# Kernel tuning notes

Measured on AMD Instinct MI355X. Metric: run time of the kernel, lower is better.

The kernel has to match this reference:

```python
import jax, jax.numpy as jnp
import numpy as np

D_MODEL = 1024
NUM_HEADS = 16
D_K = D_MODEL // NUM_HEADS
ROPE_BASE = 10000.0


def _rotate_half(x):
    # interleaved pairs: (x0, x1) -> (-x1, x0)
    x1 = x[..., ::2]
    x2 = x[..., 1::2]
    return jnp.stack((-x2, x1), axis=-1).reshape(x.shape)


def _rope(q, k):
    seq_len = q.shape[-2]
    freqs = ROPE_BASE ** (jnp.arange(0, D_K, 2, dtype=q.dtype) / D_K)  # [D_K/2]
    angles = jnp.arange(seq_len, dtype=q.dtype)[:, None] / freqs[None, :]  # [S, D_K/2]
    sin = jnp.repeat(jnp.sin(angles), 2, axis=-1)[None, None]  # [1,1,S,D_K]
    cos = jnp.repeat(jnp.cos(angles), 2, axis=-1)[None, None]
    return q * cos + _rotate_half(q) * sin, k * cos + _rotate_half(k) * sin


def setup_inputs() -> dict:
    key = jax.random.key(0)
    ks = jax.random.split(key, 9)
    B, S, D = 2, 2048, D_MODEL
    s = 1.0 / np.sqrt(D)
    inp = {
        "x": jax.random.normal(ks[0], (B, S, D), dtype=jnp.float32),
        "wq": jax.random.uniform(ks[1], (D, D), jnp.float32, -s, s),
        "bq": jax.random.uniform(ks[2], (D,), jnp.float32, -s, s),
        "wk": jax.random.uniform(ks[3], (D, D), jnp.float32, -s, s),
        "bk": jax.random.uniform(ks[4], (D,), jnp.float32, -s, s),
        "wv": jax.random.uniform(ks[5], (D, D), jnp.float32, -s, s),
        "bv": jax.random.uniform(ks[6], (D,), jnp.float32, -s, s),
        "wo": jax.random.uniform(ks[7], (D, D), jnp.float32, -s, s),
        "bo": jax.random.uniform(ks[8], (D,), jnp.float32, -s, s),
    }
    return inp


def reference(x, wq, bq, wk, bk, wv, bv, wo, bo):
    B, S, D = x.shape
    H, dk = NUM_HEADS, D_K
    # torch Linear: y = x @ W.T + b
    Q = (x @ wq.T + bq).reshape(B, S, H, dk).transpose(0, 2, 1, 3)  # [B,H,S,dk]
    K = (x @ wk.T + bk).reshape(B, S, H, dk).transpose(0, 2, 1, 3)
    V = (x @ wv.T + bv).reshape(B, S, H, dk).transpose(0, 2, 1, 3)
    Q, K = _rope(Q, K)
    score = jnp.einsum("bhqd,bhkd->bhqk", Q, K) / jnp.sqrt(jnp.asarray(dk, x.dtype))
    attn_w = jax.nn.softmax(score, axis=-1)
    out = jnp.einsum("bhqk,bhkd->bhqd", attn_w, V)  # [B,H,S,dk]
    out = out.transpose(0, 2, 1, 3).reshape(B, S, D)
    return out @ wo.T + bo
```

## Files before the change

### kernel.cpp

```cpp
#include <hip/hip_runtime.h>
#include <hip/hip_bf16.h>
#include <math.h>

typedef __bf16 bf16_t;
typedef __bf16 bf16x4_t __attribute__((ext_vector_type(4)));
typedef __bf16 bf16x8_t __attribute__((ext_vector_type(8)));
typedef float  f32x4_t  __attribute__((ext_vector_type(4)));

#define SEQ 2048
#define DM  1024
#define NH  16
#define DK  64
#define ROPE_C 0.4152410118609203f
#define EXP_C (1.4426950408889634f / 8.0f)

#define GLD16(gp, lp) \
  __builtin_amdgcn_global_load_lds((__attribute__((address_space(1))) const void*)(gp), \
                                   (__attribute__((address_space(3))) void*)(lp), 16, 0, 0)

__global__ __launch_bounds__(256)
void prep_kernel(const float* __restrict__ x,  const float* __restrict__ wq,
                 const float* __restrict__ wk, const float* __restrict__ wv,
                 const float* __restrict__ wo, bf16_t* __restrict__ dst,
                 float2* __restrict__ lut) {
  if (blockIdx.x < 8192) {
    int i = blockIdx.x * 256 + threadIdx.x;
    const float* s;
    if (i < 1048576) {
      s = x + (size_t)i * 4;
    } else {
      int j = i - 1048576;
      int w = j >> 18;
      const float* base = (w == 0) ? wq : (w == 1) ? wk : (w == 2) ? wv : wo;
      s = base + (size_t)(j & 262143) * 4;
    }
    float4 v = *(const float4*)s;
    bf16x4_t o;
    o.x = (bf16_t)v.x; o.y = (bf16_t)v.y; o.z = (bf16_t)v.z; o.w = (bf16_t)v.w;
    ((bf16x4_t*)dst)[i] = o;
  } else {
    int i = (blockIdx.x - 8192) * 256 + threadIdx.x;
    int s = i >> 5, f = i & 31;
    float ang = (float)s * exp2f(-ROPE_C * (float)f);
    float sn, cs;
    sincosf(ang, &sn, &cs);
    lut[i] = make_float2(sn, cs);
  }
}

__global__ __launch_bounds__(256, 3)
void gemm_qkv(const bf16_t* __restrict__ A, const bf16_t* __restrict__ Wq,
              const bf16_t* __restrict__ Wk, const bf16_t* __restrict__ Wv,
              const float* __restrict__ bq, const float* __restrict__ bk,
              const float* __restrict__ bv, const float2* __restrict__ lut,
              bf16_t* __restrict__ Qb, bf16_t* __restrict__ Kb,
              bf16_t* __restrict__ Vtb) {
  const int K = 1024;
  __shared__ bf16_t As[128 * 64];
  __shared__ bf16_t Bs[128 * 64];

  const int tid  = threadIdx.x;
  const int w    = tid >> 6;
  const int lane = tid & 63;
  const int quad = lane >> 4;
  const int lrow = lane & 15;
  const int wm = (w >> 1) * 64, wn = (w & 1) * 64;

  const int srow8 = lane >> 3;
  const int scolz = (((lane & 7) ^ (lane >> 3)) * 8);

  const int id   = blockIdx.x;
  const int xcd  = id & 7;
  const int rank = id >> 3;
  const int isV  = rank >= 64;

  const bf16_t* Ablk;
  const bf16_t* Bblk;
  int bmQK = 0, bnl = 0, isK = 0, bmF = 0, bnT = 0;
  if (!isV) {
    const int q = xcd * 64 + rank;
    bmQK = q >> 4;
    const int bn = q & 15;
    isK = bn >> 3;
    bnl = bn & 7;
    Ablk = A + (size_t)(bmQK * 128) * K;
    Bblk = (isK ? Wk : Wq) + (size_t)(bnl * 128) * K;
  } else {
    const int v = xcd * 32 + (rank - 64);
    bnT = v >> 3;
    bmF = v & 7;
    Ablk = Wv + (size_t)(bmF * 128) * K;
    Bblk = A + (size_t)(bnT * 128) * K;
  }

  f32x4_t acc[4][4] = {};

  for (int k0 = 0; k0 < K; k0 += 64) {
#pragma unroll
    for (int i = 0; i < 4; i++) {
      GLD16(&Ablk[(size_t)(w * 32 + i * 8 + srow8) * K + k0 + scolz], &As[(w * 32 + i * 8) * 64]);
      GLD16(&Bblk[(size_t)(w * 32 + i * 8 + srow8) * K + k0 + scolz], &Bs[(w * 32 + i * 8) * 64]);
    }
    __syncthreads();

#pragma unroll
    for (int kk = 0; kk < 2; kk++) {
      const int gsw = (((kk << 2) | quad) ^ (lrow & 7)) * 8;
      bf16x8_t af[4], bf[4];
#pragma unroll
      for (int mi = 0; mi < 4; mi++)
        af[mi] = *(const bf16x8_t*)(&As[(wm + mi * 16 + lrow) * 64 + gsw]);
#pragma unroll
      for (int ni = 0; ni < 4; ni++)
        bf[ni] = *(const bf16x8_t*)(&Bs[(wn + ni * 16 + lrow) * 64 + gsw]);
#pragma unroll
      for (int mi = 0; mi < 4; mi++)
#pragma unroll
        for (int ni = 0; ni < 4; ni++)
          acc[mi][ni] = __builtin_amdgcn_mfma_f32_16x16x32_bf16(af[mi], bf[ni], acc[mi][ni], 0, 0, 0);
    }
    __syncthreads();
  }

  if (!isV) {
    const int brow = bmQK * 128 + wm;
    const int cbase = bnl * 128 + wn;
    const float* bias = isK ? bk : bq;
    bf16_t* D = isK ? Kb : Qb;

#pragma unroll
    for (int ni = 0; ni < 4; ni++) {
      const int col = cbase + ni * 16 + lrow;
      const float bvv = bias[col];
      const int t = col & 63;
      const int h = col >> 6;
      const int fidx = t >> 1;
#pragma unroll
      for (int mi = 0; mi < 4; mi++) {
        f32x4_t v = acc[mi][ni];
#pragma unroll
        for (int r = 0; r < 4; r++) {
          const int row = brow + mi * 16 + quad * 4 + r;
          const int s = row & (SEQ - 1);
          float val = v[r] + bvv;
          const float2 sc = lut[s * 32 + fidx];
          const float pv = __shfl_xor(val, 1);
          val = (t & 1) ? (val * sc.y + pv * sc.x) : (val * sc.y - pv * sc.x);
          const int b = row >> 11;
          const size_t o = (((size_t)(b * NH + h) * SEQ) + s) * DK + t;
          D[o] = (bf16_t)val;
        }
      }
    }
  } else {
    const int fbase = bmF * 128 + wm;
    const int tbase = bnT * 128 + wn;

#pragma unroll
    for (int ni = 0; ni < 4; ni++) {
      const int t = tbase + ni * 16 + lrow;
      const int b = t >> 11;
      const int s = t & (SEQ - 1);
#pragma unroll
      for (int mi = 0; mi < 4; mi++) {
        f32x4_t v = acc[mi][ni];
        const int f = fbase + mi * 16 + quad * 4;
        const int h = f >> 6, d = f & 63;
#pragma unroll
        for (int r = 0; r < 4; r++)
          Vtb[((size_t)((b * NH + h) * DK + d + r)) * SEQ + s] = (bf16_t)(v[r] + bv[f + r]);
      }
    }
  }
}

__global__ __launch_bounds__(256)
void gemm_out(const bf16_t* __restrict__ A, const bf16_t* __restrict__ Bw,
              const float* __restrict__ bias, float* __restrict__ D) {
  const int K = 1024;
  __shared__ bf16_t As[128 * 64];
  __shared__ bf16_t Bs[64 * 64];

  const int tid  = threadIdx.x;
  const int w    = tid >> 6;
  const int lane = tid & 63;
  const int quad = lane >> 4;
  const int lrow = lane & 15;
  const int wm = (w >> 1) * 64, wn = (w & 1) * 32;

  const int srow8 = lane >> 3;
  const int scolz = (((lane & 7) ^ (lane >> 3)) * 8);

  const int id  = blockIdx.x;
  const int swz = (id & 7) * 64 + (id >> 3);
  const int bm  = swz >> 4;
  const int bn  = swz & 15;

  const bf16_t* Ablk = A  + (size_t)(bm * 128) * K;
  const bf16_t* Bblk = Bw + (size_t)(bn * 64) * K;

  f32x4_t acc[4][2] = {};

  for (int k0 = 0; k0 < K; k0 += 64) {
#pragma unroll
    for (int i = 0; i < 4; i++)
      GLD16(&Ablk[(size_t)(w * 32 + i * 8 + srow8) * K + k0 + scolz], &As[(w * 32 + i * 8) * 64]);
#pragma unroll
    for (int i = 0; i < 2; i++)
      GLD16(&Bblk[(size_t)(w * 16 + i * 8 + srow8) * K + k0 + scolz], &Bs[(w * 16 + i * 8) * 64]);
    __syncthreads();

#pragma unroll
    for (int kk = 0; kk < 2; kk++) {
      const int gsw = (((kk << 2) | quad) ^ (lrow & 7)) * 8;
      bf16x8_t af[4], bf[2];
#pragma unroll
      for (int mi = 0; mi < 4; mi++)
        af[mi] = *(const bf16x8_t*)(&As[(wm + mi * 16 + lrow) * 64 + gsw]);
#pragma unroll
      for (int ni = 0; ni < 2; ni++)
        bf[ni] = *(const bf16x8_t*)(&Bs[(wn + ni * 16 + lrow) * 64 + gsw]);
#pragma unroll
      for (int mi = 0; mi < 4; mi++)
#pragma unroll
        for (int ni = 0; ni < 2; ni++)
          acc[mi][ni] = __builtin_amdgcn_mfma_f32_16x16x32_bf16(af[mi], bf[ni], acc[mi][ni], 0, 0, 0);
    }
    __syncthreads();
  }

#pragma unroll
  for (int ni = 0; ni < 2; ni++) {
    const int col = bn * 64 + wn + ni * 16 + lrow;
    const float bvv = bias[col];
#pragma unroll
    for (int mi = 0; mi < 4; mi++) {
      f32x4_t v = acc[mi][ni];
#pragma unroll
      for (int r = 0; r < 4; r++) {
        const int row = bm * 128 + wm + mi * 16 + quad * 4 + r;
        D[(size_t)row * DM + col] = v[r] + bvv;
      }
    }
  }
}

__global__ __launch_bounds__(256, 2)
void attn_kernel(const bf16_t* __restrict__ Q, const bf16_t* __restrict__ K,
                 const bf16_t* __restrict__ Vt, bf16_t* __restrict__ AO) {
  __shared__ bf16_t Ks[128 * 64];
  __shared__ bf16_t Vs[64 * 128];

  const int tid  = threadIdx.x;
  const int w    = tid >> 6;
  const int lane = tid & 63;
  const int quad = lane >> 4;
  const int lrow = lane & 15;

  const int id  = blockIdx.x;
  const int swz = (id & 7) * 64 + (id >> 3);
  const int bh  = swz >> 4;
  const int q0  = (swz & 15) * 128 + w * 32;

  const bf16_t* Qh  = Q  + (size_t)bh * SEQ * DK;
  const bf16_t* Kh  = K  + (size_t)bh * SEQ * DK;
  const bf16_t* Vth = Vt + (size_t)bh * DK * SEQ;

  bf16x8_t qfA[2], qfB[2];
#pragma unroll
  for (int c = 0; c < 2; c++) {
    bf16x8_t ta = *(const bf16x8_t*)(&Qh[(size_t)(q0 + lrow) * DK + c * 32 + quad * 8]);
    bf16x8_t tb = *(const bf16x8_t*)(&Qh[(size_t)(q0 + 16 + lrow) * DK + c * 32 + quad * 8]);
#pragma unroll
    for (int i = 0; i < 8; i++) {
      ta[i] = (bf16_t)((float)ta[i] * EXP_C);
      tb[i] = (bf16_t)((float)tb[i] * EXP_C);
    }
    qfA[c] = ta; qfB[c] = tb;
  }

  f32x4_t accA[4] = {}, accB[4] = {};
  float lsumA = 0.f, lsumB = 0.f;

  const int krow = tid >> 1;
  const int kcol = (tid & 1) * 32;
  const int kg0  = (tid & 1) * 4;
  const int ksw  = krow & 7;
  const int kwr  = krow * 64;
  const int kw0 = kwr + (((kg0 + 0) ^ ksw) << 3);
  const int kw1 = kwr + (((kg0 + 1) ^ ksw) << 3);
  const int kw2 = kwr + (((kg0 + 2) ^ ksw) << 3);
  const int kw3 = kwr + (((kg0 + 3) ^ ksw) << 3);

  const int vrow = tid >> 2;
  const int vcol = (tid & 3) * 32;
  const int vG   = (tid & 3) * 4;
  const int vsw  = vrow & 15;
  const int vwr  = vrow * 128;
  const int vw0 = vwr + (((vG + 0) ^ vsw) << 3);
  const int vw1 = vwr + (((vG + 1) ^ vsw) << 3);
  const int vw2 = vwr + (((vG + 2) ^ vsw) << 3);
  const int vw3 = vwr + (((vG + 3) ^ vsw) << 3);

  uint4 kr0 = *(const uint4*)(&Kh[(size_t)krow * DK + kcol]);
  uint4 kr1 = *(const uint4*)(&Kh[(size_t)krow * DK + kcol + 8]);
  uint4 kr2 = *(const uint4*)(&Kh[(size_t)krow * DK + kcol + 16]);
  uint4 kr3 = *(const uint4*)(&Kh[(size_t)krow * DK + kcol + 24]);
  uint4 vr0 = *(const uint4*)(&Vth[(size_t)vrow * SEQ + vcol]);
  uint4 vr1 = *(const uint4*)(&Vth[(size_t)vrow * SEQ + vcol + 8]);
  uint4 vr2 = *(const uint4*)(&Vth[(size_t)vrow * SEQ + vcol + 16]);
  uint4 vr3 = *(const uint4*)(&Vth[(size_t)vrow * SEQ + vcol + 24]);

  for (int kt = 0; kt < SEQ / 128; ++kt) {
    *(uint4*)(&Ks[kw0]) = kr0;
    *(uint4*)(&Ks[kw1]) = kr1;
    *(uint4*)(&Ks[kw2]) = kr2;
    *(uint4*)(&Ks[kw3]) = kr3;
    *(uint2*)(&Vs[vw0])     = make_uint2(vr0.x, vr0.y);
    *(uint2*)(&Vs[vw1])     = make_uint2(vr0.z, vr0.w);
    *(uint2*)(&Vs[vw2])     = make_uint2(vr1.x, vr1.y);
    *(uint2*)(&Vs[vw3])     = make_uint2(vr1.z, vr1.w);
    *(uint2*)(&Vs[vw0 + 4]) = make_uint2(vr2.x, vr2.y);
    *(uint2*)(&Vs[vw1 + 4]) = make_uint2(vr2.z, vr2.w);
    *(uint2*)(&Vs[vw2 + 4]) = make_uint2(vr3.x, vr3.y);
    *(uint2*)(&Vs[vw3 + 4]) = make_uint2(vr3.z, vr3.w);
    __syncthreads();

    if (kt + 1 < SEQ / 128) {
      const int kb = (kt + 1) * 128;
      kr0 = *(const uint4*)(&Kh[(size_t)(kb + krow) * DK + kcol]);
      kr1 = *(const uint4*)(&Kh[(size_t)(kb + krow) * DK + kcol + 8]);
      kr2 = *(const uint4*)(&Kh[(size_t)(kb + krow) * DK + kcol + 16]);
      kr3 = *(const uint4*)(&Kh[(size_t)(kb + krow) * DK + kcol + 24]);
      vr0 = *(const uint4*)(&Vth[(size_t)vrow * SEQ + kb + vcol]);
      vr1 = *(const uint4*)(&Vth[(size_t)vrow * SEQ + kb + vcol + 8]);
      vr2 = *(const uint4*)(&Vth[(size_t)vrow * SEQ + kb + vcol + 16]);
      vr3 = *(const uint4*)(&Vth[(size_t)vrow * SEQ + kb + vcol + 24]);
    }

    __builtin_amdgcn_s_setprio(1);
#pragma unroll
    for (int c2 = 0; c2 < 4; ++c2) {
      uint2 pkA[2], pkB[2];
#pragma unroll
      for (int kk2 = 0; kk2 < 2; ++kk2) {
        const int kk = c2 * 2 + kk2;
        const int krd = (kk * 16 + lrow) * 64;
        bf16x8_t kf0 = *(const bf16x8_t*)(&Ks[krd + ((quad       ^ (lrow & 7)) << 3)]);
        bf16x8_t kf1 = *(const bf16x8_t*)(&Ks[krd + (((quad + 4) ^ (lrow & 7)) << 3)]);
        f32x4_t zA = {}, zB = {};
        zA = __builtin_amdgcn_mfma_f32_16x16x32_bf16(kf0, qfA[0], zA, 0, 0, 0);
        zA = __builtin_amdgcn_mfma_f32_16x16x32_bf16(kf1, qfA[1], zA, 0, 0, 0);
        zB = __builtin_amdgcn_mfma_f32_16x16x32_bf16(kf0, qfB[0], zB, 0, 0, 0);
        zB = __builtin_amdgcn_mfma_f32_16x16x32_bf16(kf1, qfB[1], zB, 0, 0, 0);
        const float a0 = __builtin_amdgcn_exp2f(zA[0]), a1 = __builtin_amdgcn_exp2f(zA[1]);
        const float a2 = __builtin_amdgcn_exp2f(zA[2]), a3 = __builtin_amdgcn_exp2f(zA[3]);
        const float b0 = __builtin_amdgcn_exp2f(zB[0]), b1 = __builtin_amdgcn_exp2f(zB[1]);
        const float b2 = __builtin_amdgcn_exp2f(zB[2]), b3 = __builtin_amdgcn_exp2f(zB[3]);
        lsumA += (a0 + a1) + (a2 + a3);
        lsumB += (b0 + b1) + (b2 + b3);
        pkA[kk2].x = __builtin_amdgcn_perm(__builtin_bit_cast(unsigned, a1),
                                           __builtin_bit_cast(unsigned, a0), 0x07060302u);
        pkA[kk2].y = __builtin_amdgcn_perm(__builtin_bit_cast(unsigned, a3),
                                           __builtin_bit_cast(unsigned, a2), 0x07060302u);
        pkB[kk2].x = __builtin_amdgcn_perm(__builtin_bit_cast(unsigned, b1),
                                           __builtin_bit_cast(unsigned, b0), 0x07060302u);
        pkB[kk2].y = __builtin_amdgcn_perm(__builtin_bit_cast(unsigned, b3),
                                           __builtin_bit_cast(unsigned, b2), 0x07060302u);
      }
      uint4 pfuA, pfuB;
      pfuA.x = pkA[0].x; pfuA.y = pkA[0].y; pfuA.z = pkA[1].x; pfuA.w = pkA[1].y;
      pfuB.x = pkB[0].x; pfuB.y = pkB[0].y; pfuB.z = pkB[1].x; pfuB.w = pkB[1].y;
      bf16x8_t pfA = __builtin_bit_cast(bf16x8_t, pfuA);
      bf16x8_t pfB = __builtin_bit_cast(bf16x8_t, pfuB);
#pragma unroll
      for (int nt = 0; nt < 4; ++nt) {
        bf16x8_t vf = *(const bf16x8_t*)(
            &Vs[(nt * 16 + lrow) * 128 + ((((c2 << 2) | quad) ^ lrow) << 3)]);
        accA[nt] = __builtin_amdgcn_mfma_f32_16x16x32_bf16(pfA, vf, accA[nt], 0, 0, 0);
        accB[nt] = __builtin_amdgcn_mfma_f32_16x16x32_bf16(pfB, vf, accB[nt], 0, 0, 0);
      }
    }
    __builtin_amdgcn_s_setprio(0);
    __syncthreads();
  }

  lsumA += __shfl_xor(lsumA, 16);
  lsumA += __shfl_xor(lsumA, 32);
  lsumB += __shfl_xor(lsumB, 16);
  lsumB += __shfl_xor(lsumB, 32);
  float linvA[4], linvB[4];
#pragma unroll
  for (int r = 0; r < 4; r++) {
    linvA[r] = 1.0f / __shfl(lsumA, quad * 4 + r);
    linvB[r] = 1.0f / __shfl(lsumB, quad * 4 + r);
  }

  const int b = bh >> 4, h = bh & 15;
#pragma unroll
  for (int nt = 0; nt < 4; nt++)
#pragma unroll
    for (int r = 0; r < 4; r++) {
      const int rowA = q0 + quad * 4 + r;
      const int rowB = q0 + 16 + quad * 4 + r;
      const float va = accA[nt][r] * linvA[r];
      const float vb = accB[nt][r] * linvB[r];
      AO[((size_t)(b * SEQ + rowA)) * DM + h * DK + nt * 16 + lrow] = (bf16_t)va;
      AO[((size_t)(b * SEQ + rowB)) * DM + h * DK + nt * 16 + lrow] = (bf16_t)vb;
    }
}

extern "C" void kernel_launch(void* const* d_in, const int* in_sizes, int n_in,
                              void* d_out, int out_size, void* d_ws, size_t ws_size,
                              hipStream_t stream) {
  const float* x  = (const float*)d_in[0];
  const float* wq = (const float*)d_in[1];
  const float* bq = (const float*)d_in[2];
  const float* wk = (const float*)d_in[3];
  const float* bk = (const float*)d_in[4];
  const float* wv = (const float*)d_in[5];
  const float* bv = (const float*)d_in[6];
  const float* wo = (const float*)d_in[7];
  const float* bo = (const float*)d_in[8];
  float* out = (float*)d_out;

  char* ws = (char*)d_ws;
  bf16_t* xb   = (bf16_t*)(ws);
  bf16_t* wqb  = (bf16_t*)(ws + 8388608);
  bf16_t* wkb  = (bf16_t*)(ws + 10485760);
  bf16_t* wvb  = (bf16_t*)(ws + 12582912);
  bf16_t* wob  = (bf16_t*)(ws + 14680064);
  bf16_t* Qb   = (bf16_t*)(ws + 16777216);
  bf16_t* Kb   = (bf16_t*)(ws + 25165824);
  bf16_t* Vtb  = (bf16_t*)(ws + 33554432);
  bf16_t* AOb  = (bf16_t*)(ws + 41943040);
  float2* lut  = (float2*)(ws + 50331648);

  prep_kernel<<<8448, 256, 0, stream>>>(x, wq, wk, wv, wo, xb, lut);

  gemm_qkv<<<768, 256, 0, stream>>>(xb, wqb, wkb, wvb, bq, bk, bv, lut, Qb, Kb, Vtb);

  attn_kernel<<<512, 256, 0, stream>>>(Qb, Kb, Vtb, AOb);

  gemm_out<<<512, 256, 0, stream>>>(AOb, wob, bo, out);
}
```

Baseline: 171.7 us.

## Double per-block query tile in attention to 256 rows, halving grid

Each wave in the attention kernel now handles 64 query rows in four 16-row groups instead of 32, so a block covers 256 queries and the grid shrinks from 512 to 256 blocks. Each K/V tile staged in shared memory is reused by twice as many queries, which halves global K/V traffic and block-level sync overhead. The cost is roughly double the accumulator and Q-fragment registers; the occupancy hint in launch bounds is dropped. With only 256 blocks on a 256-CU part, each CU gets about one block, so latency hiding may suffer.

```diff
diff --git a/kernel.cpp b/kernel.cpp
--- a/kernel.cpp
+++ b/kernel.cpp
@@ -245,7 +245,7 @@
   }
 }
 
-__global__ __launch_bounds__(256, 2)
+__global__ __launch_bounds__(256)
 void attn_kernel(const bf16_t* __restrict__ Q, const bf16_t* __restrict__ K,
                  const bf16_t* __restrict__ Vt, bf16_t* __restrict__ AO) {
   __shared__ bf16_t Ks[128 * 64];
@@ -258,29 +258,33 @@
   const int lrow = lane & 15;
 
   const int id  = blockIdx.x;
-  const int swz = (id & 7) * 64 + (id >> 3);
-  const int bh  = swz >> 4;
-  const int q0  = (swz & 15) * 128 + w * 32;
+  const int swz = (id & 7) * 32 + (id >> 3);
+  const int bh  = swz >> 3;
+  const int q0  = (swz & 7) * 256 + w * 64;
 
   const bf16_t* Qh  = Q  + (size_t)bh * SEQ * DK;
   const bf16_t* Kh  = K  + (size_t)bh * SEQ * DK;
   const bf16_t* Vth = Vt + (size_t)bh * DK * SEQ;
 
-  bf16x8_t qfA[2], qfB[2];
+  bf16x8_t qfA[2], qfB[2], qfC[2], qfD[2];
 #pragma unroll
   for (int c = 0; c < 2; c++) {
-    bf16x8_t ta = *(const bf16x8_t*)(&Qh[(size_t)(q0 + lrow) * DK + c * 32 + quad * 8]);
+    bf16x8_t ta = *(const bf16x8_t*)(&Qh[(size_t)(q0 +      lrow) * DK + c * 32 + quad * 8]);
     bf16x8_t tb = *(const bf16x8_t*)(&Qh[(size_t)(q0 + 16 + lrow) * DK + c * 32 + quad * 8]);
+    bf16x8_t tc = *(const bf16x8_t*)(&Qh[(size_t)(q0 + 32 + lrow) * DK + c * 32 + quad * 8]);
+    bf16x8_t td = *(const bf16x8_t*)(&Qh[(size_t)(q0 + 48 + lrow) * DK + c * 32 + quad * 8]);
 #pragma unroll
     for (int i = 0; i < 8; i++) {
       ta[i] = (bf16_t)((float)ta[i] * EXP_C);
       tb[i] = (bf16_t)((float)tb[i] * EXP_C);
-    }
-    qfA[c] = ta; qfB[c] = tb;
-  }
-
-  f32x4_t accA[4] = {}, accB[4] = {};
-  float lsumA = 0.f, lsumB = 0.f;
+      tc[i] = (bf16_t)((float)tc[i] * EXP_C);
+      td[i] = (bf16_t)((float)td[i] * EXP_C);
+    }
+    qfA[c] = ta; qfB[c] = tb; qfC[c] = tc; qfD[c] = td;
+  }
+
+  f32x4_t accA[4] = {}, accB[4] = {}, accC[4] = {}, accD[4] = {};
+  float lsumA = 0.f, lsumB = 0.f, lsumC = 0.f, lsumD = 0.f;
 
   const int krow = tid >> 1;
   const int kcol = (tid & 1) * 32;
@@ -341,24 +345,34 @@
     __builtin_amdgcn_s_setprio(1);
 #pragma unroll
     for (int c2 = 0; c2 < 4; ++c2) {
-      uint2 pkA[2], pkB[2];
+      uint2 pkA[2], pkB[2], pkC[2], pkD[2];
 #pragma unroll
       for (int kk2 = 0; kk2 < 2; ++kk2) {
         const int kk = c2 * 2 + kk2;
         const int krd = (kk * 16 + lrow) * 64;
         bf16x8_t kf0 = *(const bf16x8_t*)(&Ks[krd + ((quad       ^ (lrow & 7)) << 3)]);
         bf16x8_t kf1 = *(const bf16x8_t*)(&Ks[krd + (((quad + 4) ^ (lrow & 7)) << 3)]);
-        f32x4_t zA = {}, zB = {};
+        f32x4_t zA = {}, zB = {}, zC = {}, zD = {};
         zA = __builtin_amdgcn_mfma_f32_16x16x32_bf16(kf0, qfA[0], zA, 0, 0, 0);
         zA = __builtin_amdgcn_mfma_f32_16x16x32_bf16(kf1, qfA[1], zA, 0, 0, 0);
         zB = __builtin_amdgcn_mfma_f32_16x16x32_bf16(kf0, qfB[0], zB, 0, 0, 0);
         zB = __builtin_amdgcn_mfma_f32_16x16x32_bf16(kf1, qfB[1], zB, 0, 0, 0);
+        zC = __builtin_amdgcn_mfma_f32_16x16x32_bf16(kf0, qfC[0], zC, 0, 0, 0);
+        zC = __builtin_amdgcn_mfma_f32_16x16x32_bf16(kf1, qfC[1], zC, 0, 0, 0);
+        zD = __builtin_amdgcn_mfma_f32_16x16x32_bf16(kf0, qfD[0], zD, 0, 0, 0);
+        zD = __builtin_amdgcn_mfma_f32_16x16x32_bf16(kf1, qfD[1], zD, 0, 0, 0);
         const float a0 = __builtin_amdgcn_exp2f(zA[0]), a1 = __builtin_amdgcn_exp2f(zA[1]);
         const float a2 = __builtin_amdgcn_exp2f(zA[2]), a3 = __builtin_amdgcn_exp2f(zA[3]);
         const float b0 = __builtin_amdgcn_exp2f(zB[0]), b1 = __builtin_amdgcn_exp2f(zB[1]);
         const float b2 = __builtin_amdgcn_exp2f(zB[2]), b3 = __builtin_amdgcn_exp2f(zB[3]);
+        const float c0 = __builtin_amdgcn_exp2f(zC[0]), c1 = __builtin_amdgcn_exp2f(zC[1]);
+        const float c2f = __builtin_amdgcn_exp2f(zC[2]), c3 = __builtin_amdgcn_exp2f(zC[3]);
+        const float d0 = __builtin_amdgcn_exp2f(zD[0]), d1 = __builtin_amdgcn_exp2f(zD[1]);
+        const float d2 = __builtin_amdgcn_exp2f(zD[2]), d3 = __builtin_amdgcn_exp2f(zD[3]);
         lsumA += (a0 + a1) + (a2 + a3);
         lsumB += (b0 + b1) + (b2 + b3);
+        lsumC += (c0 + c1) + (c2f + c3);
+        lsumD += (d0 + d1) + (d2 + d3);
         pkA[kk2].x = __builtin_amdgcn_perm(__builtin_bit_cast(unsigned, a1),
                                            __builtin_bit_cast(unsigned, a0), 0x07060302u);
         pkA[kk2].y = __builtin_amdgcn_perm(__builtin_bit_cast(unsigned, a3),
@@ -367,33 +381,49 @@
                                            __builtin_bit_cast(unsigned, b0), 0x07060302u);
         pkB[kk2].y = __builtin_amdgcn_perm(__builtin_bit_cast(unsigned, b3),
                                            __builtin_bit_cast(unsigned, b2), 0x07060302u);
+        pkC[kk2].x = __builtin_amdgcn_perm(__builtin_bit_cast(unsigned, c1),
+                                           __builtin_bit_cast(unsigned, c0), 0x07060302u);
+        pkC[kk2].y = __builtin_amdgcn_perm(__builtin_bit_cast(unsigned, c3),
+                                           __builtin_bit_cast(unsigned, c2f), 0x07060302u);
+        pkD[kk2].x = __builtin_amdgcn_perm(__builtin_bit_cast(unsigned, d1),
+                                           __builtin_bit_cast(unsigned, d0), 0x07060302u);
+        pkD[kk2].y = __builtin_amdgcn_perm(__builtin_bit_cast(unsigned, d3),
+                                           __builtin_bit_cast(unsigned, d2), 0x07060302u);
       }
-      uint4 pfuA, pfuB;
+      uint4 pfuA, pfuB, pfuC, pfuD;
       pfuA.x = pkA[0].x; pfuA.y = pkA[0].y; pfuA.z = pkA[1].x; pfuA.w = pkA[1].y;
       pfuB.x = pkB[0].x; pfuB.y = pkB[0].y; pfuB.z = pkB[1].x; pfuB.w = pkB[1].y;
+      pfuC.x = pkC[0].x; pfuC.y = pkC[0].y; pfuC.z = pkC[1].x; pfuC.w = pkC[1].y;
+      pfuD.x = pkD[0].x; pfuD.y = pkD[0].y; pfuD.z = pkD[1].x; pfuD.w = pkD[1].y;
       bf16x8_t pfA = __builtin_bit_cast(bf16x8_t, pfuA);
       bf16x8_t pfB = __builtin_bit_cast(bf16x8_t, pfuB);
+      bf16x8_t pfC = __builtin_bit_cast(bf16x8_t, pfuC);
+      bf16x8_t pfD = __builtin_bit_cast(bf16x8_t, pfuD);
 #pragma unroll
       for (int nt = 0; nt < 4; ++nt) {
         bf16x8_t vf = *(const bf16x8_t*)(
             &Vs[(nt * 16 + lrow) * 128 + ((((c2 << 2) | quad) ^ lrow) << 3)]);
         accA[nt] = __builtin_amdgcn_mfma_f32_16x16x32_bf16(pfA, vf, accA[nt], 0, 0, 0);
         accB[nt] = __builtin_amdgcn_mfma_f32_16x16x32_bf16(pfB, vf, accB[nt], 0, 0, 0);
+        accC[nt] = __builtin_amdgcn_mfma_f32_16x16x32_bf16(pfC, vf, accC[nt], 0, 0, 0);
+        accD[nt] = __builtin_amdgcn_mfma_f32_16x16x32_bf16(pfD, vf, accD[nt], 0, 0, 0);
       }
     }
     __builtin_amdgcn_s_setprio(0);
     __syncthreads();
   }
 
-  lsumA += __shfl_xor(lsumA, 16);
-  lsumA += __shfl_xor(lsumA, 32);
-  lsumB += __shfl_xor(lsumB, 16);
-  lsumB += __shfl_xor(lsumB, 32);
-  float linvA[4], linvB[4];
+  lsumA += __shfl_xor(lsumA, 16);  lsumA += __shfl_xor(lsumA, 32);
+  lsumB += __shfl_xor(lsumB, 16);  lsumB += __shfl_xor(lsumB, 32);
+  lsumC += __shfl_xor(lsumC, 16);  lsumC += __shfl_xor(lsumC, 32);
+  lsumD += __shfl_xor(lsumD, 16);  lsumD += __shfl_xor(lsumD, 32);
+  float linvA[4], linvB[4], linvC[4], linvD[4];
 #pragma unroll
   for (int r = 0; r < 4; r++) {
     linvA[r] = 1.0f / __shfl(lsumA, quad * 4 + r);
     linvB[r] = 1.0f / __shfl(lsumB, quad * 4 + r);
+    linvC[r] = 1.0f / __shfl(lsumC, quad * 4 + r);
+    linvD[r] = 1.0f / __shfl(lsumD, quad * 4 + r);
   }
 
   const int b = bh >> 4, h = bh & 15;
@@ -401,12 +431,15 @@
   for (int nt = 0; nt < 4; nt++)
 #pragma unroll
     for (int r = 0; r < 4; r++) {
-      const int rowA = q0 + quad * 4 + r;
-      const int rowB = q0 + 16 + quad * 4 + r;
-      const float va = accA[nt][r] * linvA[r];
-      const float vb = accB[nt][r] * linvB[r];
-      AO[((size_t)(b * SEQ + rowA)) * DM + h * DK + nt * 16 + lrow] = (bf16_t)va;
-      AO[((size_t)(b * SEQ + rowB)) * DM + h * DK + nt * 16 + lrow] = (bf16_t)vb;
+      const int ra = q0 +      quad * 4 + r;
+      const int rb = q0 + 16 + quad * 4 + r;
+      const int rc = q0 + 32 + quad * 4 + r;
+      const int rd = q0 + 48 + quad * 4 + r;
+      const size_t cb = h * DK + nt * 16 + lrow;
+      AO[((size_t)(b * SEQ + ra)) * DM + cb] = (bf16_t)(accA[nt][r] * linvA[r]);
+      AO[((size_t)(b * SEQ + rb)) * DM + cb] = (bf16_t)(accB[nt][r] * linvB[r]);
+      AO[((size_t)(b * SEQ + rc)) * DM + cb] = (bf16_t)(accC[nt][r] * linvC[r]);
+      AO[((size_t)(b * SEQ + rd)) * DM + cb] = (bf16_t)(accD[nt][r] * linvD[r]);
     }
 }
 
@@ -440,7 +473,7 @@
 
   gemm_qkv<<<768, 256, 0, stream>>>(xb, wqb, wkb, wvb, bq, bk, bv, lut, Qb, Kb, Vtb);
 
-  attn_kernel<<<512, 256, 0, stream>>>(Qb, Kb, Vtb, AOb);
+  attn_kernel<<<256, 256, 0, stream>>>(Qb, Kb, Vtb, AOb);
 
   gemm_out<<<512, 256, 0, stream>>>(AOb, wob, bo, out);
 }
```

Result: slower. 186.1 us (+8.4%).
